# Kernel optimization log

Hardware: AMD Instinct MI355X
Metric: run time of the kernel (lower is better)

The kernel has to match this reference:

```python
import jax, jax.numpy as jnp
import numpy as np


def setup_inputs() -> dict:
    key = jax.random.key(0)
    k1, k2 = jax.random.split(key)
    B, C, H, W = 4, 64, 256, 512
    l_fmap = jax.random.normal(k1, (B, C, H, W), dtype=jnp.float32)
    r_fmap = jax.random.normal(k2, (B, C, H, W), dtype=jnp.float32)
    return {"l_fmap": l_fmap, "r_fmap": r_fmap, "max_disp": 48}


def reference(l_fmap, r_fmap, max_disp):
    # l_fmap, r_fmap: [B, C, H, W]
    w = l_fmap.shape[-1]
    # zero-pad right fmap along width by max_disp on both sides
    r_pad = jnp.pad(r_fmap, ((0, 0), (0, 0), (0, 0), (max_disp, max_disp)))
    planes = []
    for d in range(-max_disp, max_disp + 1):  # fixed small loop over 2*max_disp+1 disparities
        begin = max_disp - d
        # channel-mean of elementwise correlation at shift d -> [B, H, W]
        planes.append(jnp.mean(l_fmap * r_pad[:, :, :, begin:begin + w], axis=1))
    # cost volume: [B, 2*max_disp+1, H, W]
    return jnp.stack(planes, axis=1)
```

## Files before the change

kernel.cpp:

```cpp
#include <hip/hip_runtime.h>


#define B_  4
#define C_  64
#define H_  256
#define W_  512
#define MD  48
#define ND  97
#define WT  64
#define RT  160
#define HW  (H_ * W_)

typedef __attribute__((ext_vector_type(8))) short  short8;
typedef __attribute__((ext_vector_type(4))) float  floatx4;

__device__ __forceinline__ unsigned f2bf(float f) {
    unsigned u = __builtin_bit_cast(unsigned, f);
    return (u + 0x7FFFu + ((u >> 16) & 1u)) >> 16;
}

union SM {
    struct {
        short l[WT * C_];
        short r[RT * C_];
    } st;
    float out_s[ND * 68];
};

__global__ __launch_bounds__(256, 4) void cost_volume_kernel(
    const float* __restrict__ L, const float* __restrict__ R,
    float* __restrict__ out)
{
    __shared__ SM sm;
    const int tid  = threadIdx.x;
    const int w0   = blockIdx.x * WT;
    const int h    = blockIdx.y;
    const int b    = blockIdx.z;
    const int lane = tid & 63;
    const int wv   = tid >> 6;

    const size_t in_base = (((size_t)b * C_) * H_ + h) * (size_t)W_;

    {
        const int wl = tid & 63;
        const int m  = wl & 15, wq = wl >> 4;
        const float* lp = L + in_base + w0 + wl;
        #pragma unroll
        for (int i = 0; i < 2; ++i) {
            const int cc = (tid >> 6) + 4 * i;
            unsigned d[4];
            #pragma unroll
            for (int jj = 0; jj < 4; ++jj) {
                float f0 = lp[(size_t)(cc * 8 + 2 * jj)     * HW] * 0.015625f;
                float f1 = lp[(size_t)(cc * 8 + 2 * jj + 1) * HW] * 0.015625f;
                d[jj] = f2bf(f0) | (f2bf(f1) << 16);
            }
            const int chunk = (wq * 8 + cc) * 16 + m;
            *((uint4*)&sm.st.l[chunk * 8]) = make_uint4(d[0], d[1], d[2], d[3]);
        }
    }

    #pragma unroll
    for (int wc = 0; wc < 3; ++wc) {
        const int ul = wc * 64 + (tid & 63);
        if (ul < RT) {
            const int  ug = w0 - MD + ul;
            const bool ok = ((unsigned)ug < (unsigned)W_);
            const float* rp = R + in_base + ug;
            const int m = ul & 15, uq = ul >> 4;
            #pragma unroll
            for (int i = 0; i < 2; ++i) {
                const int cc = (tid >> 6) + 4 * i;
                unsigned d[4];
                #pragma unroll
                for (int jj = 0; jj < 4; ++jj) {
                    float f0 = ok ? rp[(size_t)(cc * 8 + 2 * jj)     * HW] : 0.0f;
                    float f1 = ok ? rp[(size_t)(cc * 8 + 2 * jj + 1) * HW] : 0.0f;
                    d[jj] = f2bf(f0) | (f2bf(f1) << 16);
                }
                const int chunk = (uq * 8 + cc) * 16 + m;
                *((uint4*)&sm.st.r[chunk * 8]) = make_uint4(d[0], d[1], d[2], d[3]);
            }
        }
    }
    __syncthreads();

    const int q   = lane >> 4;
    const int m16 = lane & 15;
    const short8* lv = (const short8*)sm.st.l;
    const short8* rv = (const short8*)sm.st.r;

    const short8 a0 = lv[(wv * 8 +     q) * 16 + m16];
    const short8 a1 = lv[(wv * 8 + 4 + q) * 16 + m16];

    floatx4 acc[7];
    #pragma unroll
    for (int t = 0; t < 7; ++t) {
        const short8 b0 = rv[((wv + t) * 8 +     q) * 16 + m16];
        const short8 b1 = rv[((wv + t) * 8 + 4 + q) * 16 + m16];
        floatx4 c = {0.f, 0.f, 0.f, 0.f};
        c = __builtin_amdgcn_mfma_f32_16x16x32_bf16(a0, b0, c, 0, 0, 0);
        c = __builtin_amdgcn_mfma_f32_16x16x32_bf16(a1, b1, c, 0, 0, 0);
        acc[t] = c;
    }
    __syncthreads();

    #pragma unroll
    for (int t = 0; t < 7; ++t) {
        #pragma unroll
        for (int r = 0; r < 4; ++r) {
            const int ml    = q * 4 + r;
            const int d_idx = ml - m16 + 96 - 16 * t;
            if ((unsigned)d_idx <= 96u) {
                const int w_local = wv * 16 + ml;
                sm.out_s[d_idx * 68 + w_local] = acc[t][r];
            }
        }
    }
    __syncthreads();

    float* ob = out + (((size_t)b * ND) * H_ + h) * (size_t)W_ + w0;
    for (int i = tid; i < ND * WT; i += 256) {
        const int dr = i >> 6, wl = i & 63;
        ob[(size_t)dr * HW + wl] = sm.out_s[dr * 68 + wl];
    }
}

extern "C" void kernel_launch(void* const* d_in, const int* in_sizes, int n_in,
                              void* d_out, int out_size, void* d_ws, size_t ws_size,
                              hipStream_t stream) {
    const float* L = (const float*)d_in[0];
    const float* R = (const float*)d_in[1];
    float* out = (float*)d_out;
    (void)in_sizes; (void)n_in; (void)d_ws; (void)ws_size; (void)out_size;
    dim3 grid(W_ / WT, H_, B_);
    hipLaunchKernelGGL(cost_volume_kernel, grid, dim3(256), 0, stream, L, R, out);
}
```

Measured before the change: 413.5 us.

## Process a full image row per block to remove halo reloads of right features

```diff
diff --git a/kernel.cpp b/kernel.cpp
--- a/kernel.cpp
+++ b/kernel.cpp
@@ -5,11 +5,11 @@
 #define C_  64
 #define H_  256
 #define W_  512
-#define MD  48
 #define ND  97
-#define WT  64
-#define RT  160
+#define NWT 32
 #define HW  (H_ * W_)
+#define PAD 513
+#define CH0 49
 
 typedef __attribute__((ext_vector_type(8))) short  short8;
 typedef __attribute__((ext_vector_type(4))) float  floatx4;
@@ -21,108 +21,101 @@
 
 union SM {
     struct {
-        short l[WT * C_];
-        short r[RT * C_];
+        short l[W_ * C_];
+        short r[W_ * C_];
     } st;
-    float out_s[ND * 68];
+    float out_s[CH0 * PAD];
 };
 
-__global__ __launch_bounds__(256, 4) void cost_volume_kernel(
+__global__ __launch_bounds__(1024, 4) void cost_volume_kernel(
     const float* __restrict__ L, const float* __restrict__ R,
     float* __restrict__ out)
 {
     __shared__ SM sm;
-    const int tid  = threadIdx.x;
-    const int w0   = blockIdx.x * WT;
-    const int h    = blockIdx.y;
-    const int b    = blockIdx.z;
-    const int lane = tid & 63;
-    const int wv   = tid >> 6;
-
+    const int tid = threadIdx.x;
+    const int h   = blockIdx.x;
+    const int b   = blockIdx.y;
     const size_t in_base = (((size_t)b * C_) * H_ + h) * (size_t)W_;
 
     {
-        const int wl = tid & 63;
+        const int wl = tid & 511;
+        const int ch = tid >> 9;
         const int m  = wl & 15, wq = wl >> 4;
-        const float* lp = L + in_base + w0 + wl;
+        const float* lp = L + in_base + wl;
+        const float* rp = R + in_base + wl;
         #pragma unroll
-        for (int i = 0; i < 2; ++i) {
-            const int cc = (tid >> 6) + 4 * i;
-            unsigned d[4];
+        for (int i = 0; i < 4; ++i) {
+            const int cc = ch + 2 * i;
+            unsigned dl[4], dr[4];
             #pragma unroll
             for (int jj = 0; jj < 4; ++jj) {
-                float f0 = lp[(size_t)(cc * 8 + 2 * jj)     * HW] * 0.015625f;
-                float f1 = lp[(size_t)(cc * 8 + 2 * jj + 1) * HW] * 0.015625f;
-                d[jj] = f2bf(f0) | (f2bf(f1) << 16);
+                float l0 = lp[(size_t)(cc * 8 + 2 * jj)     * HW] * 0.015625f;
+                float l1 = lp[(size_t)(cc * 8 + 2 * jj + 1) * HW] * 0.015625f;
+                float r0 = rp[(size_t)(cc * 8 + 2 * jj)     * HW];
+                float r1 = rp[(size_t)(cc * 8 + 2 * jj + 1) * HW];
+                dl[jj] = f2bf(l0) | (f2bf(l1) << 16);
+                dr[jj] = f2bf(r0) | (f2bf(r1) << 16);
             }
             const int chunk = (wq * 8 + cc) * 16 + m;
-            *((uint4*)&sm.st.l[chunk * 8]) = make_uint4(d[0], d[1], d[2], d[3]);
-        }
-    }
-
-    #pragma unroll
-    for (int wc = 0; wc < 3; ++wc) {
-        const int ul = wc * 64 + (tid & 63);
-        if (ul < RT) {
-            const int  ug = w0 - MD + ul;
-            const bool ok = ((unsigned)ug < (unsigned)W_);
-            const float* rp = R + in_base + ug;
-            const int m = ul & 15, uq = ul >> 4;
-            #pragma unroll
-            for (int i = 0; i < 2; ++i) {
-                const int cc = (tid >> 6) + 4 * i;
-                unsigned d[4];
-                #pragma unroll
-                for (int jj = 0; jj < 4; ++jj) {
-                    float f0 = ok ? rp[(size_t)(cc * 8 + 2 * jj)     * HW] : 0.0f;
-                    float f1 = ok ? rp[(size_t)(cc * 8 + 2 * jj + 1) * HW] : 0.0f;
-                    d[jj] = f2bf(f0) | (f2bf(f1) << 16);
-                }
-                const int chunk = (uq * 8 + cc) * 16 + m;
-                *((uint4*)&sm.st.r[chunk * 8]) = make_uint4(d[0], d[1], d[2], d[3]);
-            }
+            *((uint4*)&sm.st.l[chunk * 8]) = make_uint4(dl[0], dl[1], dl[2], dl[3]);
+            *((uint4*)&sm.st.r[chunk * 8]) = make_uint4(dr[0], dr[1], dr[2], dr[3]);
         }
     }
     __syncthreads();
 
-    const int q   = lane >> 4;
-    const int m16 = lane & 15;
+    const int lane = tid & 63;
+    const int wv   = tid >> 6;
+    const int q    = lane >> 4, m16 = lane & 15;
     const short8* lv = (const short8*)sm.st.l;
     const short8* rv = (const short8*)sm.st.r;
 
-    const short8 a0 = lv[(wv * 8 +     q) * 16 + m16];
-    const short8 a1 = lv[(wv * 8 + 4 + q) * 16 + m16];
+    floatx4 acc[2][7];
+    #pragma unroll
+    for (int half = 0; half < 2; ++half) {
+        const int wt = wv + 16 * half;
+        const short8 a0 = lv[(wt * 8 +     q) * 16 + m16];
+        const short8 a1 = lv[(wt * 8 + 4 + q) * 16 + m16];
+        #pragma unroll
+        for (int t = 0; t < 7; ++t) {
+            floatx4 c = {0.f, 0.f, 0.f, 0.f};
+            const int ut = wt + t - 3;
+            if ((unsigned)ut < (unsigned)NWT) {
+                const short8 b0 = rv[(ut * 8 +     q) * 16 + m16];
+                const short8 b1 = rv[(ut * 8 + 4 + q) * 16 + m16];
+                c = __builtin_amdgcn_mfma_f32_16x16x32_bf16(a0, b0, c, 0, 0, 0);
+                c = __builtin_amdgcn_mfma_f32_16x16x32_bf16(a1, b1, c, 0, 0, 0);
+            }
+            acc[half][t] = c;
+        }
+    }
 
-    floatx4 acc[7];
+    float* ob = out + (((size_t)b * ND) * H_ + h) * (size_t)W_;
+    int lo = 0;
     #pragma unroll
-    for (int t = 0; t < 7; ++t) {
-        const short8 b0 = rv[((wv + t) * 8 +     q) * 16 + m16];
-        const short8 b1 = rv[((wv + t) * 8 + 4 + q) * 16 + m16];
-        floatx4 c = {0.f, 0.f, 0.f, 0.f};
-        c = __builtin_amdgcn_mfma_f32_16x16x32_bf16(a0, b0, c, 0, 0, 0);
-        c = __builtin_amdgcn_mfma_f32_16x16x32_bf16(a1, b1, c, 0, 0, 0);
-        acc[t] = c;
-    }
-    __syncthreads();
-
-    #pragma unroll
-    for (int t = 0; t < 7; ++t) {
+    for (int ck = 0; ck < 2; ++ck) {
+        const int cnt = ck ? (ND - CH0) : CH0;
+        __syncthreads();
         #pragma unroll
-        for (int r = 0; r < 4; ++r) {
-            const int ml    = q * 4 + r;
-            const int d_idx = ml - m16 + 96 - 16 * t;
-            if ((unsigned)d_idx <= 96u) {
-                const int w_local = wv * 16 + ml;
-                sm.out_s[d_idx * 68 + w_local] = acc[t][r];
+        for (int half = 0; half < 2; ++half) {
+            const int wt = wv + 16 * half;
+            #pragma unroll
+            for (int t = 0; t < 7; ++t) {
+                #pragma unroll
+                for (int r = 0; r < 4; ++r) {
+                    const int ml    = q * 4 + r;
+                    const int d_idx = ml - m16 + 96 - 16 * t;
+                    const int drel  = d_idx - lo;
+                    if ((unsigned)drel < (unsigned)cnt)
+                        sm.out_s[drel * PAD + wt * 16 + ml] = acc[half][t][r];
+                }
             }
         }
-    }
-    __syncthreads();
-
-    float* ob = out + (((size_t)b * ND) * H_ + h) * (size_t)W_ + w0;
-    for (int i = tid; i < ND * WT; i += 256) {
-        const int dr = i >> 6, wl = i & 63;
-        ob[(size_t)dr * HW + wl] = sm.out_s[dr * 68 + wl];
+        __syncthreads();
+        for (int i = tid; i < cnt * W_; i += 1024) {
+            const int pr = i >> 9, w = i & 511;
+            ob[(size_t)(lo + pr) * HW + w] = sm.out_s[pr * PAD + w];
+        }
+        lo += CH0;
     }
 }
 
@@ -133,6 +126,6 @@
     const float* R = (const float*)d_in[1];
     float* out = (float*)d_out;
     (void)in_sizes; (void)n_in; (void)d_ws; (void)ws_size; (void)out_size;
-    dim3 grid(W_ / WT, H_, B_);
-    hipLaunchKernelGGL(cost_volume_kernel, grid, dim3(256), 0, stream, L, R, out);
+    dim3 grid(H_, B_);
+    hipLaunchKernelGGL(cost_volume_kernel, grid, dim3(1024), 0, stream, L, R, out);
 }
```

Result: faster. 386.6 us (-6.5%).
